# Kernel tuning notes

Measured on AMD Instinct MI355X. Metric: run time of the kernel, lower is better.

## Reference

```python
import jax, jax.numpy as jnp
import numpy as np

B, S, H, F, V, MAX_OOV = 128, 512, 1024, 512, 50000, 50


def setup_inputs() -> dict:
    key = jax.random.key(0)
    ks = jax.random.split(key, 20)
    r = lambda i, shp, s=0.02: (jax.random.normal(ks[i], shp, jnp.float32) * s)
    return dict(
        input=jax.random.randint(ks[0], (B,), 0, V),
        hidden=jax.random.normal(ks[1], (1, B, H), jnp.float32) * 0.1,
        encoder_outputs=jax.random.normal(ks[2], (B, S, H), jnp.float32) * 0.1,
        x_padding_masks=jnp.ones((B, S), jnp.float32),
        len_oov=jax.random.randint(ks[3], (B,), 0, MAX_OOV),
        coverage_vector=jnp.zeros((B, S), jnp.float32),
        ref2tgt=jax.random.randint(ks[4], (B, S), 0, V + MAX_OOV),
        emb=r(5, (V, F)),
        W_ih=r(6, (3 * H, F)), W_hh=r(7, (3 * H, H)),
        b_ih=jnp.zeros(3 * H, jnp.float32), b_hh=jnp.zeros(3 * H, jnp.float32),
        e2v1_w=r(8, (F, H)), e2v1_b=jnp.zeros(F, jnp.float32),
        e2v2_w=r(9, (V, F)), e2v2_b=jnp.zeros(V, jnp.float32),
        fc_w=r(10, (H, 2 * H)), fc_b=jnp.zeros(H, jnp.float32),
        wgen_w=r(11, (1, 2 * H + F)), wgen_b=jnp.zeros(1, jnp.float32),
        att_Wh=r(12, (H, H)), att_Ws=r(13, (H, H)),
        att_wc=r(14, (H,)), att_b=jnp.zeros(H, jnp.float32), att_v=r(15, (H,)),
    )


def reference(input, hidden, encoder_outputs, x_padding_masks, len_oov,
              coverage_vector, ref2tgt, emb, W_ih, W_hh, b_ih, b_hh,
              e2v1_w, e2v1_b, e2v2_w, e2v2_b, fc_w, fc_b, wgen_w, wgen_b,
              att_Wh, att_Ws, att_wc, att_b, att_v):
    # embedding lookup (dropout is identity at inference)
    emb_x = emb[input]  # [B, F]

    # --- additive (Bahdanau) attention with coverage ---
    s = hidden[0]  # [B, H] (n_layers == 1)
    feat = jnp.tanh(
        jnp.einsum('bsh,kh->bsk', encoder_outputs, att_Wh)
        + (s @ att_Ws.T)[:, None, :]
        + coverage_vector[:, :, None] * att_wc
        + att_b)  # [B, S, H]
    e = jnp.einsum('bsh,h->bs', feat, att_v)  # [B, S]
    a = jax.nn.softmax(e, axis=1) * x_padding_masks
    a = a / (jnp.sum(a, axis=1, keepdims=True))  # [B, S] renormalized attn
    coverage_new = coverage_vector + a
    context = jnp.einsum('bs,bsh->bh', a, encoder_outputs)  # [B, H]
    h_att = jnp.concatenate([s, context], axis=-1) @ fc_w.T + fc_b  # [B, H]

    # --- single-step GRU (PyTorch gate order r, z, n) ---
    gi = emb_x @ W_ih.T + b_ih  # [B, 3H]
    gh = h_att @ W_hh.T + b_hh  # [B, 3H]
    i_r, i_z, i_n = jnp.split(gi, 3, axis=-1)
    h_r, h_z, h_n = jnp.split(gh, 3, axis=-1)
    r = jax.nn.sigmoid(i_r + h_r)
    z = jax.nn.sigmoid(i_z + h_z)
    n = jnp.tanh(i_n + r * h_n)
    h_new = (1.0 - z) * n + z * h_att  # [B, H]

    # --- vocab distribution ---
    out1 = h_new @ e2v1_w.T + e2v1_b  # [B, F]
    p_vocab = jax.nn.softmax(out1 @ e2v2_w.T + e2v2_b, axis=1)  # [B, V]

    # --- pointer-generator mixing ---
    x_gen = jnp.concatenate([context, h_new, emb_x], axis=-1)  # [B, 2H+F]
    p_gen = jax.nn.sigmoid(x_gen @ wgen_w.T + wgen_b)[:, 0]  # [B]
    p_gen = jnp.clip(p_gen, 0.001, 0.999)
    p_vocab_w = p_gen[:, None] * p_vocab  # [B, V]
    attn_w = (1.0 - p_gen)[:, None] * a  # [B, S]
    p_ext = jnp.concatenate([p_vocab_w, jnp.zeros((B, MAX_OOV), p_vocab_w.dtype)], axis=1)
    rows = jnp.arange(B)[:, None]
    final = p_ext.at[rows, ref2tgt].add(attn_w)  # scatter_add over extended vocab

    return final, h_new[None], coverage_new, a
```

## Files before the change

### kernel.cpp

```cpp
#include <hip/hip_runtime.h>
#include <math.h>

#define B_   128
#define S_   512
#define H_   1024
#define F_   512
#define V_   50000
#define OOV_ 50
#define EV_  (V_ + OOV_)

#define BM 128
#define BN 128
#define BK 64

#define BM2 256
#define BN2 256
#define BK2 64

typedef __attribute__((ext_vector_type(8))) __bf16 bf16x8;
typedef __attribute__((ext_vector_type(4))) __bf16 bf16x4;
typedef __attribute__((ext_vector_type(4))) float  f32x4;

__device__ __forceinline__ void gload_lds16(const void* g, void* lds) {
  __builtin_amdgcn_global_load_lds(
      (const __attribute__((address_space(1))) unsigned int*)g,
      (__attribute__((address_space(3))) unsigned int*)lds, 16, 0, 0);
}

__device__ __forceinline__ float fast_tanh(float x) {
  float v = fminf(fmaxf(x, -15.f), 15.f);
  float t = __expf(2.f * v);
  return 1.f - 2.f / (t + 1.f);
}

__global__ __launch_bounds__(256)
void cast_both_kernel(const float* __restrict__ enc, __bf16* __restrict__ enc_h,
                      const float* __restrict__ wh, __bf16* __restrict__ wh_h)
{
  const size_t n_enc = (size_t)B_ * S_ * H_;
  const size_t n_tot = n_enc + (size_t)H_ * H_;
  for (size_t i = ((size_t)blockIdx.x * 256 + threadIdx.x) * 8; i < n_tot;
       i += (size_t)gridDim.x * 256 * 8) {
    const float* in; __bf16* out; size_t j;
    if (i < n_enc) { in = enc; out = enc_h; j = i; }
    else           { in = wh;  out = wh_h;  j = i - n_enc; }
    float4 a = *(const float4*)(in + j);
    float4 b = *(const float4*)(in + j + 4);
    bf16x8 o;
    o[0] = (__bf16)a.x; o[1] = (__bf16)a.y; o[2] = (__bf16)a.z; o[3] = (__bf16)a.w;
    o[4] = (__bf16)b.x; o[5] = (__bf16)b.y; o[6] = (__bf16)b.z; o[7] = (__bf16)b.w;
    *(bf16x8*)(out + j) = o;
  }
}

__global__ __launch_bounds__(256)
void gemm_splitk(const float* __restrict__ A, const float* __restrict__ W,
                 float* __restrict__ partial, int N, int K, int KS)
{
  __shared__ float As[128 * 68];
  __shared__ float Ws[32 * 68];
  const int tid = threadIdx.x;
  const int n0 = blockIdx.x * 32;
  const int p  = blockIdx.y;
  const int tx = tid & 7, ty = tid >> 3;
  const int lr = tid >> 4, lc4 = (tid & 15) * 4;
  float acc[4][4] = {};
  const int kend = p * KS + KS;
  for (int k0 = p * KS; k0 < kend; k0 += 64) {
#pragma unroll
    for (int pp = 0; pp < 8; ++pp)
      *(float4*)(As + (pp * 16 + lr) * 68 + lc4) =
          *(const float4*)(A + (size_t)(pp * 16 + lr) * K + k0 + lc4);
#pragma unroll
    for (int pp = 0; pp < 2; ++pp)
      *(float4*)(Ws + (pp * 16 + lr) * 68 + lc4) =
          *(const float4*)(W + (size_t)(n0 + pp * 16 + lr) * K + k0 + lc4);
    __syncthreads();
#pragma unroll
    for (int kk = 0; kk < 16; ++kk) {
      float4 av[4], wv[4];
#pragma unroll
      for (int i = 0; i < 4; i++) av[i] = *(const float4*)(As + (ty * 4 + i) * 68 + kk * 4);
#pragma unroll
      for (int j = 0; j < 4; j++) wv[j] = *(const float4*)(Ws + (tx * 4 + j) * 68 + kk * 4);
#pragma unroll
      for (int i = 0; i < 4; i++)
#pragma unroll
        for (int j = 0; j < 4; j++) {
          acc[i][j] = fmaf(av[i].x, wv[j].x, acc[i][j]);
          acc[i][j] = fmaf(av[i].y, wv[j].y, acc[i][j]);
          acc[i][j] = fmaf(av[i].z, wv[j].z, acc[i][j]);
          acc[i][j] = fmaf(av[i].w, wv[j].w, acc[i][j]);
        }
    }
    __syncthreads();
  }
#pragma unroll
  for (int i = 0; i < 4; i++)
#pragma unroll
    for (int j = 0; j < 4; j++)
      partial[((size_t)p * 128 + ty * 4 + i) * N + n0 + tx * 4 + j] = acc[i][j];
}

__global__ __launch_bounds__(256)
void gemm_splitk_cat(const float* __restrict__ A1, const float* __restrict__ A2,
                     const float* __restrict__ W, float* __restrict__ partial,
                     int N, int K, int KS)
{
  __shared__ float As[128 * 68];
  __shared__ float Ws[32 * 68];
  const int tid = threadIdx.x;
  const int n0 = blockIdx.x * 32;
  const int p  = blockIdx.y;
  const int tx = tid & 7, ty = tid >> 3;
  const int lr = tid >> 4, lc4 = (tid & 15) * 4;
  const float* A = (p * KS < 1024) ? A1 : A2;
  const int kbase = (p * KS < 1024) ? 0 : 1024;
  float acc[4][4] = {};
  const int kend = p * KS + KS;
  for (int k0 = p * KS; k0 < kend; k0 += 64) {
#pragma unroll
    for (int pp = 0; pp < 8; ++pp)
      *(float4*)(As + (pp * 16 + lr) * 68 + lc4) =
          *(const float4*)(A + (size_t)(pp * 16 + lr) * 1024 + (k0 - kbase) + lc4);
#pragma unroll
    for (int pp = 0; pp < 2; ++pp)
      *(float4*)(Ws + (pp * 16 + lr) * 68 + lc4) =
          *(const float4*)(W + (size_t)(n0 + pp * 16 + lr) * K + k0 + lc4);
    __syncthreads();
#pragma unroll
    for (int kk = 0; kk < 16; ++kk) {
      float4 av[4], wv[4];
#pragma unroll
      for (int i = 0; i < 4; i++) av[i] = *(const float4*)(As + (ty * 4 + i) * 68 + kk * 4);
#pragma unroll
      for (int j = 0; j < 4; j++) wv[j] = *(const float4*)(Ws + (tx * 4 + j) * 68 + kk * 4);
#pragma unroll
      for (int i = 0; i < 4; i++)
#pragma unroll
        for (int j = 0; j < 4; j++) {
          acc[i][j] = fmaf(av[i].x, wv[j].x, acc[i][j]);
          acc[i][j] = fmaf(av[i].y, wv[j].y, acc[i][j]);
          acc[i][j] = fmaf(av[i].z, wv[j].z, acc[i][j]);
          acc[i][j] = fmaf(av[i].w, wv[j].w, acc[i][j]);
        }
    }
    __syncthreads();
  }
#pragma unroll
  for (int i = 0; i < 4; i++)
#pragma unroll
    for (int j = 0; j < 4; j++)
      partial[((size_t)p * 128 + ty * 4 + i) * N + n0 + tx * 4 + j] = acc[i][j];
}

__global__ __launch_bounds__(256)
void gemm_splitk_gather(const int* __restrict__ input, const float* __restrict__ emb,
                        const float* __restrict__ W, float* __restrict__ partial,
                        int N, int K, int KS)
{
  __shared__ float As[128 * 68];
  __shared__ float Ws[32 * 68];
  const int tid = threadIdx.x;
  const int n0 = blockIdx.x * 32;
  const int p  = blockIdx.y;
  const int tx = tid & 7, ty = tid >> 3;
  const int lr = tid >> 4, lc4 = (tid & 15) * 4;
  float acc[4][4] = {};
  const int kend = p * KS + KS;
  for (int k0 = p * KS; k0 < kend; k0 += 64) {
#pragma unroll
    for (int pp = 0; pp < 8; ++pp) {
      int row = input[pp * 16 + lr];
      *(float4*)(As + (pp * 16 + lr) * 68 + lc4) =
          *(const float4*)(emb + (size_t)row * K + k0 + lc4);
    }
#pragma unroll
    for (int pp = 0; pp < 2; ++pp)
      *(float4*)(Ws + (pp * 16 + lr) * 68 + lc4) =
          *(const float4*)(W + (size_t)(n0 + pp * 16 + lr) * K + k0 + lc4);
    __syncthreads();
#pragma unroll
    for (int kk = 0; kk < 16; ++kk) {
      float4 av[4], wv[4];
#pragma unroll
      for (int i = 0; i < 4; i++) av[i] = *(const float4*)(As + (ty * 4 + i) * 68 + kk * 4);
#pragma unroll
      for (int j = 0; j < 4; j++) wv[j] = *(const float4*)(Ws + (tx * 4 + j) * 68 + kk * 4);
#pragma unroll
      for (int i = 0; i < 4; i++)
#pragma unroll
        for (int j = 0; j < 4; j++) {
          acc[i][j] = fmaf(av[i].x, wv[j].x, acc[i][j]);
          acc[i][j] = fmaf(av[i].y, wv[j].y, acc[i][j]);
          acc[i][j] = fmaf(av[i].z, wv[j].z, acc[i][j]);
          acc[i][j] = fmaf(av[i].w, wv[j].w, acc[i][j]);
        }
    }
    __syncthreads();
  }
#pragma unroll
  for (int i = 0; i < 4; i++)
#pragma unroll
    for (int j = 0; j < 4; j++)
      partial[((size_t)p * 128 + ty * 4 + i) * N + n0 + tx * 4 + j] = acc[i][j];
}

__global__ __launch_bounds__(256)
void reduce_partial(const float* __restrict__ partial, const float* __restrict__ bias,
                    float* __restrict__ C, int N, int P)
{
  int idx = blockIdx.x * 256 + threadIdx.x;
  int n = idx % N;
  float s = bias ? bias[n] : 0.f;
  for (int p = 0; p < P; ++p) s += partial[(size_t)p * 128 * N + idx];
  C[idx] = s;
}

__global__ __launch_bounds__(256)
void reduce_partial_bf16(const float* __restrict__ partial, const float* __restrict__ bias,
                         __bf16* __restrict__ C, int N, int P)
{
  int idx = blockIdx.x * 256 + threadIdx.x;
  int n = idx % N;
  float s = bias ? bias[n] : 0.f;
  for (int p = 0; p < P; ++p) s += partial[(size_t)p * 128 * N + idx];
  C[idx] = (__bf16)s;
}

__global__ __launch_bounds__(512, 1)
void feat_mfma256_kernel(const __bf16* __restrict__ enc, const __bf16* __restrict__ Wh,
                         const float* __restrict__ sws, const float* __restrict__ cov,
                         const float* __restrict__ wcv, const float* __restrict__ ab,
                         const float* __restrict__ av_, float* __restrict__ e_part)
{
  __shared__ __attribute__((aligned(16))) __bf16 As[2][BM2 * BK2];
  __shared__ __attribute__((aligned(16))) __bf16 Bs[2][BN2 * BK2];
  const int tid  = threadIdx.x;
  const int lane = tid & 63, wid = tid >> 6;
  const int wr = wid >> 2, wc = wid & 3;
  const int bid = blockIdx.x;
  const int swz = (bid & 7) * 128 + (bid >> 3);
  const int mt = swz >> 2, nt = swz & 3;
  const int bs0 = mt * BM2;
  const int n0  = nt * BN2;
  const int b   = bs0 >> 9;

  const int scb = ((tid & 7) * 16) ^ (((tid >> 3) & 7) << 4);
  const __bf16* aP[4]; const __bf16* bP[4]; int ldsO[4];
#pragma unroll
  for (int p = 0; p < 4; ++p) {
    int r = p * 64 + (tid >> 3);
    ldsO[p] = p * 8192 + tid * 16;
    aP[p] = enc + (size_t)(bs0 + r) * H_ + (scb >> 1);
    bP[p] = Wh  + (size_t)(n0  + r) * H_ + (scb >> 1);
  }

  const int lrow = lane & 15;
  const int kbase = (lane >> 4) << 4;
  int aO[8][2], bO[4][2];
#pragma unroll
  for (int m = 0; m < 8; ++m) {
    int row = wr * 128 + m * 16 + lrow;
    int sw = (row & 7) << 4;
#pragma unroll
    for (int kk = 0; kk < 2; ++kk)
      aO[m][kk] = row * 128 + ((kk * 64 + kbase) ^ sw);
  }
#pragma unroll
  for (int n = 0; n < 4; ++n) {
    int row = wc * 64 + n * 16 + lrow;
    int sw = (row & 7) << 4;
#pragma unroll
    for (int kk = 0; kk < 2; ++kk)
      bO[n][kk] = row * 128 + ((kk * 64 + kbase) ^ sw);
  }

  f32x4 acc[8][4];
#pragma unroll
  for (int i = 0; i < 8; i++)
#pragma unroll
    for (int j = 0; j < 4; j++) acc[i][j] = (f32x4){0.f, 0.f, 0.f, 0.f};

#define STAGE(c, ofs)                                                          \
  {                                                                            \
    _Pragma("unroll")                                                          \
    for (int p = 0; p < 4; ++p) {                                              \
      gload_lds16(aP[p] + (ofs), (char*)As[c] + ldsO[p]);                      \
      gload_lds16(bP[p] + (ofs), (char*)Bs[c] + ldsO[p]);                      \
    }                                                                          \
  }

#define COMPUTE(c)                                                             \
  {                                                                            \
    bf16x8 bfv[4][2];                                                          \
    _Pragma("unroll")                                                          \
    for (int n = 0; n < 4; ++n)                                                \
      _Pragma("unroll")                                                        \
      for (int kk = 0; kk < 2; ++kk)                                           \
        bfv[n][kk] = *(const bf16x8*)((const char*)Bs[c] + bO[n][kk]);         \
    __builtin_amdgcn_s_setprio(1);                                             \
    _Pragma("unroll")                                                          \
    for (int m = 0; m < 8; ++m) {                                              \
      bf16x8 a0 = *(const bf16x8*)((const char*)As[c] + aO[m][0]);             \
      bf16x8 a1 = *(const bf16x8*)((const char*)As[c] + aO[m][1]);             \
      _Pragma("unroll")                                                        \
      for (int n = 0; n < 4; ++n) {                                            \
        acc[m][n] = __builtin_amdgcn_mfma_f32_16x16x32_bf16(a0, bfv[n][0], acc[m][n], 0, 0, 0); \
        acc[m][n] = __builtin_amdgcn_mfma_f32_16x16x32_bf16(a1, bfv[n][1], acc[m][n], 0, 0, 0); \
      }                                                                        \
    }                                                                          \
    __builtin_amdgcn_s_setprio(0);                                             \
  }

#define VMCNT8() asm volatile("s_waitcnt vmcnt(8)" ::: "memory")
#define VMCNT0() asm volatile("s_waitcnt vmcnt(0)" ::: "memory")
#define BARRIER()                                                              \
  {                                                                            \
    __builtin_amdgcn_sched_barrier(0);                                         \
    __builtin_amdgcn_s_barrier();                                              \
    __builtin_amdgcn_sched_barrier(0);                                         \
  }

  STAGE(0, 0)
  STAGE(1, 64)

#pragma unroll 1
  for (int t2 = 0; t2 < 7; ++t2) {
    VMCNT8(); BARRIER();
    COMPUTE(0)
    BARRIER();
    STAGE(0, 128)
    VMCNT8(); BARRIER();
    COMPUTE(1)
    BARRIER();
    STAGE(1, 192)
#pragma unroll
    for (int p = 0; p < 4; ++p) { aP[p] += 128; bP[p] += 128; }
  }
  VMCNT8(); BARRIER();
  COMPUTE(0)
  BARRIER();
  VMCNT0(); BARRIER();
  COMPUTE(1)
  __syncthreads();
#undef STAGE
#undef COMPUTE
#undef VMCNT8
#undef VMCNT0
#undef BARRIER

  float rowsum[8][4];
#pragma unroll
  for (int m = 0; m < 8; m++)
#pragma unroll
    for (int j = 0; j < 4; j++) rowsum[m][j] = 0.f;

#pragma unroll
  for (int n = 0; n < 4; ++n) {
    int col_g = n0 + wc * 64 + n * 16 + (lane & 15);
    float sw   = sws[(size_t)b * H_ + col_g];
    float wc_n = wcv[col_g], ab_n = ab[col_g], av_n = av_[col_g];
#pragma unroll
    for (int m = 0; m < 8; ++m) {
#pragma unroll
      for (int j = 0; j < 4; ++j) {
        int row_l = wr * 128 + m * 16 + ((lane >> 4) << 2) + j;
        float val = acc[m][n][j] + sw + cov[bs0 + row_l] * wc_n + ab_n;
        rowsum[m][j] += fast_tanh(val) * av_n;
      }
    }
  }
#pragma unroll
  for (int m = 0; m < 8; ++m)
#pragma unroll
    for (int j = 0; j < 4; ++j) {
      float v = rowsum[m][j];
      v += __shfl_xor(v, 1);
      v += __shfl_xor(v, 2);
      v += __shfl_xor(v, 4);
      v += __shfl_xor(v, 8);
      rowsum[m][j] = v;
    }
  float (*red)[4] = (float(*)[4])As;
  if ((lane & 15) == 0) {
#pragma unroll
    for (int m = 0; m < 8; ++m)
#pragma unroll
      for (int j = 0; j < 4; ++j)
        red[wr * 128 + m * 16 + ((lane >> 4) << 2) + j][wc] = rowsum[m][j];
  }
  __syncthreads();
  if (tid < BM2)
    e_part[(size_t)nt * (B_ * S_) + bs0 + tid] =
        red[tid][0] + red[tid][1] + red[tid][2] + red[tid][3];
}

__global__ __launch_bounds__(256)
void logits_mfma_kernel(const __bf16* __restrict__ A, const float* __restrict__ W,
                        const float* __restrict__ bias, float* __restrict__ out0)
{
  __shared__ __attribute__((aligned(16))) __bf16 As[BM * BK];
  __shared__ __attribute__((aligned(16))) __bf16 Bs[BN * BK];
  const int tid  = threadIdx.x;
  const int lane = tid & 63, wid = tid >> 6;
  const int wr = wid >> 1, wcc = wid & 1;
  const int n0 = blockIdx.x * BN;

  f32x4 acc[4][4];
#pragma unroll
  for (int i = 0; i < 4; i++)
#pragma unroll
    for (int j = 0; j < 4; j++) acc[i][j] = (f32x4){0.f, 0.f, 0.f, 0.f};

  for (int k0 = 0; k0 < F_; k0 += BK) {
#pragma unroll
    for (int p = 0; p < 4; ++p) {
      int off = p * 4096 + tid * 16;
      int r = off >> 7, cb = off & 127;
      int scb = cb ^ ((r & 7) << 4);
      gload_lds16(A + (size_t)r * F_ + k0 + (scb >> 1), (char*)As + off);
    }
#pragma unroll
    for (int p = 0; p < 8; ++p) {
      int idx = p * 1024 + tid * 4;
      int r = idx >> 6, c = idx & 63;
      int row_g = n0 + r; if (row_g >= V_) row_g = V_ - 1;
      float4 f = *(const float4*)(W + (size_t)row_g * F_ + k0 + c);
      union { __bf16 h[4]; uint2 u; } t;
      t.h[0] = (__bf16)f.x; t.h[1] = (__bf16)f.y; t.h[2] = (__bf16)f.z; t.h[3] = (__bf16)f.w;
      int cb = c * 2;
      *(uint2*)((char*)Bs + r * 128 + (cb ^ ((r & 7) << 4))) = t.u;
    }
    __syncthreads();

    bf16x8 af[4][2], bfv[4][2];
#pragma unroll
    for (int m = 0; m < 4; ++m) {
      int row = wr * 64 + m * 16 + (lane & 15);
      int swz = (row & 7) << 4;
#pragma unroll
      for (int kk = 0; kk < 2; ++kk) {
        int kb = kk * 64 + ((lane >> 4) << 4);
        af[m][kk] = *(const bf16x8*)((const char*)As + row * 128 + (kb ^ swz));
      }
    }
#pragma unroll
    for (int n = 0; n < 4; ++n) {
      int row = wcc * 64 + n * 16 + (lane & 15);
      int swz = (row & 7) << 4;
#pragma unroll
      for (int kk = 0; kk < 2; ++kk) {
        int kb = kk * 64 + ((lane >> 4) << 4);
        bfv[n][kk] = *(const bf16x8*)((const char*)Bs + row * 128 + (kb ^ swz));
      }
    }
#pragma unroll
    for (int m = 0; m < 4; ++m)
#pragma unroll
      for (int n = 0; n < 4; ++n)
#pragma unroll
        for (int kk = 0; kk < 2; ++kk)
          acc[m][n] = __builtin_amdgcn_mfma_f32_16x16x32_bf16(af[m][kk], bfv[n][kk], acc[m][n], 0, 0, 0);
    __syncthreads();
  }

#pragma unroll
  for (int m = 0; m < 4; ++m) {
#pragma unroll
    for (int n = 0; n < 4; ++n) {
      int col_g = n0 + wcc * 64 + n * 16 + (lane & 15);
      if (col_g >= V_) continue;
      float bv = bias[col_g];
#pragma unroll
      for (int j = 0; j < 4; ++j) {
        int row = wr * 64 + m * 16 + ((lane >> 4) << 2) + j;
        out0[(size_t)row * EV_ + col_g] = acc[m][n][j] + bv;
      }
    }
  }
}

__global__ __launch_bounds__(512)
void softmax_a_kernel(const float* __restrict__ e_part, const float* __restrict__ mask,
                      const float* __restrict__ cov, float* __restrict__ a_ws,
                      float* __restrict__ out_a, float* __restrict__ out_cov)
{
  const int b = blockIdx.x;
  const int s = threadIdx.x;
  __shared__ float red[512];
  float e = 0.f;
  for (int kt = 0; kt < 4; ++kt) e += e_part[(size_t)kt * (B_ * S_) + b * S_ + s];
  red[s] = e;
  __syncthreads();
  for (int st = 256; st > 0; st >>= 1) {
    if (s < st) red[s] = fmaxf(red[s], red[s + st]);
    __syncthreads();
  }
  float mx = red[0];
  __syncthreads();
  float ex = expf(e - mx) * mask[b * S_ + s];
  red[s] = ex;
  __syncthreads();
  for (int st = 256; st > 0; st >>= 1) {
    if (s < st) red[s] += red[s + st];
    __syncthreads();
  }
  float a = ex / red[0];
  a_ws[b * S_ + s] = a;
  out_a[b * S_ + s] = a;
  out_cov[b * S_ + s] = cov[b * S_ + s] + a;
}

__global__ __launch_bounds__(256)
void context_kernel(const float* __restrict__ a_ws, const __bf16* __restrict__ enc,
                    float* __restrict__ ctx)
{
  const int b = blockIdx.y, q = blockIdx.x;
  const int lane = threadIdx.x & 63, w = threadIdx.x >> 6;
  const int h0 = q * 256 + lane * 4;
  __shared__ float al[S_];
  __shared__ float part[4][256];
  for (int i = threadIdx.x; i < S_; i += 256) al[i] = a_ws[b * S_ + i];
  __syncthreads();
  float acc0 = 0.f, acc1 = 0.f, acc2 = 0.f, acc3 = 0.f;
  const __bf16* ep = enc + (size_t)b * S_ * H_ + h0;
#pragma unroll 4
  for (int s = w * 128; s < w * 128 + 128; ++s) {
    bf16x4 v = *(const bf16x4*)(ep + (size_t)s * H_);
    float a = al[s];
    acc0 = fmaf(a, (float)v[0], acc0);
    acc1 = fmaf(a, (float)v[1], acc1);
    acc2 = fmaf(a, (float)v[2], acc2);
    acc3 = fmaf(a, (float)v[3], acc3);
  }
  part[w][lane * 4 + 0] = acc0;
  part[w][lane * 4 + 1] = acc1;
  part[w][lane * 4 + 2] = acc2;
  part[w][lane * 4 + 3] = acc3;
  __syncthreads();
  if (threadIdx.x < 256) {
    int o = threadIdx.x;
    ctx[b * H_ + q * 256 + o] = part[0][o] + part[1][o] + part[2][o] + part[3][o];
  }
}

__global__ __launch_bounds__(256)
void gru_kernel(const float* __restrict__ pgi, const float* __restrict__ pgh,
                const float* __restrict__ b_ih, const float* __restrict__ b_hh,
                const float* __restrict__ h_att, float* __restrict__ h_new_ws,
                float* __restrict__ out_h)
{
  int idx = blockIdx.x * 256 + threadIdx.x;
  int b = idx >> 10, h = idx & 1023;
  float ir = b_ih[h], iz = b_ih[H_ + h], in_ = b_ih[2 * H_ + h];
  float hr = b_hh[h], hz = b_hh[H_ + h], hn = b_hh[2 * H_ + h];
#pragma unroll
  for (int p = 0; p < 8; ++p) {
    const float* gp = pgi + (size_t)p * 128 * 3072 + (size_t)b * 3072;
    ir += gp[h]; iz += gp[H_ + h]; in_ += gp[2 * H_ + h];
    const float* hp = pgh + (size_t)p * 128 * 3072 + (size_t)b * 3072;
    hr += hp[h]; hz += hp[H_ + h]; hn += hp[2 * H_ + h];
  }
  float r = 1.f / (1.f + expf(-(ir + hr)));
  float z = 1.f / (1.f + expf(-(iz + hz)));
  float n = tanhf(in_ + r * hn);
  float ha = h_att[(size_t)b * H_ + h];
  float hv = (1.f - z) * n + z * ha;
  h_new_ws[idx] = hv;
  out_h[idx] = hv;
}

__global__ __launch_bounds__(512)
void stats_pgen_kernel(const float* __restrict__ logits, float* __restrict__ vmax,
                       float* __restrict__ vsum, const float* __restrict__ context,
                       const float* __restrict__ h_new, const int* __restrict__ input,
                       const float* __restrict__ emb, const float* __restrict__ wgen_w,
                       const float* __restrict__ wgen_b, float* __restrict__ pgen)
{
  __shared__ float red[512];
  if (blockIdx.x < B_) {
    int b = blockIdx.x;
    const float* row = logits + (size_t)b * EV_;
    float m = -1e30f;
    for (int v = threadIdx.x; v < V_; v += 512) m = fmaxf(m, row[v]);
    red[threadIdx.x] = m;
    __syncthreads();
    for (int st = 256; st > 0; st >>= 1) {
      if (threadIdx.x < st) red[threadIdx.x] = fmaxf(red[threadIdx.x], red[threadIdx.x + st]);
      __syncthreads();
    }
    m = red[0];
    __syncthreads();
    float ssum = 0.f;
    for (int v = threadIdx.x; v < V_; v += 512) ssum += expf(row[v] - m);
    red[threadIdx.x] = ssum;
    __syncthreads();
    for (int st = 256; st > 0; st >>= 1) {
      if (threadIdx.x < st) red[threadIdx.x] += red[threadIdx.x + st];
      __syncthreads();
    }
    if (threadIdx.x == 0) { vmax[b] = m; vsum[b] = red[0]; }
  } else {
    int b = blockIdx.x - B_;
    const float* erow = emb + (size_t)input[b] * F_;
    float acc = 0.f;
    for (int j = threadIdx.x; j < H_; j += 512) acc = fmaf(context[b * H_ + j], wgen_w[j], acc);
    for (int j = threadIdx.x; j < H_; j += 512) acc = fmaf(h_new[b * H_ + j], wgen_w[H_ + j], acc);
    for (int j = threadIdx.x; j < F_; j += 512) acc = fmaf(erow[j], wgen_w[2 * H_ + j], acc);
    red[threadIdx.x] = acc;
    __syncthreads();
    for (int st = 256; st > 0; st >>= 1) {
      if (threadIdx.x < st) red[threadIdx.x] += red[threadIdx.x + st];
      __syncthreads();
    }
    if (threadIdx.x == 0) {
      float p = 1.f / (1.f + expf(-(red[0] + wgen_b[0])));
      p = fminf(fmaxf(p, 0.001f), 0.999f);
      pgen[b] = p;
    }
  }
}

__global__ void final_kernel(float* __restrict__ out0, const float* __restrict__ vmax,
                             const float* __restrict__ vsum, const float* __restrict__ pgen)
{
  int b = blockIdx.y;
  int v = blockIdx.x * 256 + threadIdx.x;
  if (v >= EV_) return;
  float* row = out0 + (size_t)b * EV_;
  if (v < V_) row[v] = pgen[b] * expf(row[v] - vmax[b]) / vsum[b];
  else row[v] = 0.f;
}

__global__ void scatter_kernel(const int* __restrict__ ref2tgt, const float* __restrict__ a_ws,
                               const float* __restrict__ pgen, float* __restrict__ out0)
{
  int b = blockIdx.x;
  int s = threadIdx.x;
  float w = (1.f - pgen[b]) * a_ws[b * S_ + s];
  int t = ref2tgt[b * S_ + s];
  atomicAdd(&out0[(size_t)b * EV_ + t], w);
}

extern "C" void kernel_launch(void* const* d_in, const int* in_sizes, int n_in,
                              void* d_out, int out_size, void* d_ws, size_t ws_size,
                              hipStream_t stream)
{
  const int*   input   = (const int*)d_in[0];
  const float* hidden  = (const float*)d_in[1];
  const float* enc     = (const float*)d_in[2];
  const float* mask    = (const float*)d_in[3];
  const float* cov     = (const float*)d_in[5];
  const int*   ref2tgt = (const int*)d_in[6];
  const float* emb     = (const float*)d_in[7];
  const float* W_ih    = (const float*)d_in[8];
  const float* W_hh    = (const float*)d_in[9];
  const float* b_ih    = (const float*)d_in[10];
  const float* b_hh    = (const float*)d_in[11];
  const float* e2v1_w  = (const float*)d_in[12];
  const float* e2v1_b  = (const float*)d_in[13];
  const float* e2v2_w  = (const float*)d_in[14];
  const float* e2v2_b  = (const float*)d_in[15];
  const float* fc_w    = (const float*)d_in[16];
  const float* fc_b    = (const float*)d_in[17];
  const float* wgen_w  = (const float*)d_in[18];
  const float* wgen_b  = (const float*)d_in[19];
  const float* att_Wh  = (const float*)d_in[20];
  const float* att_Ws  = (const float*)d_in[21];
  const float* att_wc  = (const float*)d_in[22];
  const float* att_b   = (const float*)d_in[23];
  const float* att_v   = (const float*)d_in[24];

  char* w = (char*)d_ws;
  __bf16* enc_h  = (__bf16*)w;  w += (size_t)B_ * S_ * H_ * 2;
  __bf16* Wh_h   = (__bf16*)w;  w += (size_t)H_ * H_ * 2;
  __bf16* out1_h = (__bf16*)w;  w += (size_t)B_ * F_ * 2;
  float* sws     = (float*)w;   w += (size_t)B_ * H_ * 4;
  float* e_part  = (float*)w;   w += (size_t)8 * B_ * S_ * 4;
  float* a_ws    = (float*)w;   w += (size_t)B_ * S_ * 4;
  float* context = (float*)w;   w += (size_t)B_ * H_ * 4;
  float* h_att   = (float*)w;   w += (size_t)B_ * H_ * 4;
  float* h_new   = (float*)w;   w += (size_t)B_ * H_ * 4;
  float* pgen    = (float*)w;   w += 128 * 4;
  float* vmax    = (float*)w;   w += 128 * 4;
  float* vsum    = (float*)w;   w += 128 * 4;
  float* pA      = (float*)w;   w += (size_t)16 * 128 * 1024 * 4;
  float* pB      = (float*)w;   w += (size_t)8 * 128 * 3072 * 4;
  float* pC      = (float*)w;   w += (size_t)8 * 128 * 3072 * 4;

  float* out0    = (float*)d_out;
  float* out_h   = out0 + (size_t)B_ * EV_;
  float* out_cov = out_h + (size_t)B_ * H_;
  float* out_a   = out_cov + (size_t)B_ * S_;

  cast_both_kernel<<<4096, 256, 0, stream>>>(enc, enc_h, att_Wh, Wh_h);
  gemm_splitk<<<dim3(32, 16), 256, 0, stream>>>(hidden, att_Ws, pA, H_, H_, 64);
  reduce_partial<<<512, 256, 0, stream>>>(pA, nullptr, sws, H_, 16);
  feat_mfma256_kernel<<<dim3(1024), 512, 0, stream>>>(enc_h, Wh_h, sws, cov, att_wc, att_b, att_v, e_part);
  softmax_a_kernel<<<B_, 512, 0, stream>>>(e_part, mask, cov, a_ws, out_a, out_cov);
  context_kernel<<<dim3(4, B_), 256, 0, stream>>>(a_ws, enc_h, context);
  gemm_splitk_cat<<<dim3(32, 16), 256, 0, stream>>>(hidden, context, fc_w, pA, H_, 2 * H_, 128);
  reduce_partial<<<512, 256, 0, stream>>>(pA, fc_b, h_att, H_, 16);
  gemm_splitk_gather<<<dim3(96, 8), 256, 0, stream>>>(input, emb, W_ih, pB, 3 * H_, F_, 64);
  gemm_splitk<<<dim3(96, 8), 256, 0, stream>>>(h_att, W_hh, pC, 3 * H_, H_, 128);
  gru_kernel<<<(B_ * H_) / 256, 256, 0, stream>>>(pB, pC, b_ih, b_hh, h_att, h_new, out_h);
  gemm_splitk<<<dim3(16, 16), 256, 0, stream>>>(h_new, e2v1_w, pA, F_, H_, 64);
  reduce_partial_bf16<<<256, 256, 0, stream>>>(pA, e2v1_b, out1_h, F_, 16);
  logits_mfma_kernel<<<dim3((V_ + BN - 1) / BN), 256, 0, stream>>>(out1_h, e2v2_w, e2v2_b, out0);
  stats_pgen_kernel<<<2 * B_, 512, 0, stream>>>(out0, vmax, vsum, context, h_new, input, emb,
                                                wgen_w, wgen_b, pgen);
  final_kernel<<<dim3((EV_ + 255) / 256, B_), 256, 0, stream>>>(out0, vmax, vsum, pgen);
  scatter_kernel<<<B_, 512, 0, stream>>>(ref2tgt, a_ws, pgen, out0);
}
```

Baseline: 484.0 us.

## Split feat GEMM K-loop into fine-grained phases interleaving loads with MFMA

Restructures the attention-feature GEMM main loop into an HipKittens-style 8-phase schedule. LDS tiles are split into half-tiles, and each phase issues one small global->LDS stage, reads A fragments, then runs 16 MFMAs. The goal is to spread memory traffic evenly across compute and hide load latency better than the previous two-big-stage double buffer. It adds more barriers and lgkm waits per K step, and the handling of buffer reuse between phases is delicate.

```diff
diff --git a/kernel.cpp b/kernel.cpp
--- a/kernel.cpp
+++ b/kernel.cpp
@@ -12,10 +12,6 @@
 #define BM 128
 #define BN 128
 #define BK 64
-
-#define BM2 256
-#define BN2 256
-#define BK2 64
 
 typedef __attribute__((ext_vector_type(8))) __bf16 bf16x8;
 typedef __attribute__((ext_vector_type(4))) __bf16 bf16x4;
@@ -234,46 +230,45 @@
                          const float* __restrict__ wcv, const float* __restrict__ ab,
                          const float* __restrict__ av_, float* __restrict__ e_part)
 {
-  __shared__ __attribute__((aligned(16))) __bf16 As[2][BM2 * BK2];
-  __shared__ __attribute__((aligned(16))) __bf16 Bs[2][BN2 * BK2];
+  __shared__ __attribute__((aligned(16))) __bf16 As[2][2][128 * 64];
+  __shared__ __attribute__((aligned(16))) __bf16 Bs[2][2][128 * 64];
   const int tid  = threadIdx.x;
   const int lane = tid & 63, wid = tid >> 6;
   const int wr = wid >> 2, wc = wid & 3;
   const int bid = blockIdx.x;
   const int swz = (bid & 7) * 128 + (bid >> 3);
   const int mt = swz >> 2, nt = swz & 3;
-  const int bs0 = mt * BM2;
-  const int n0  = nt * BN2;
+  const int bs0 = mt * 256;
+  const int n0  = nt * 256;
   const int b   = bs0 >> 9;
 
   const int scb = ((tid & 7) * 16) ^ (((tid >> 3) & 7) << 4);
-  const __bf16* aP[4]; const __bf16* bP[4]; int ldsO[4];
-#pragma unroll
-  for (int p = 0; p < 4; ++p) {
-    int r = p * 64 + (tid >> 3);
-    ldsO[p] = p * 8192 + tid * 16;
-    aP[p] = enc + (size_t)(bs0 + r) * H_ + (scb >> 1);
-    bP[p] = Wh  + (size_t)(n0  + r) * H_ + (scb >> 1);
-  }
-
-  const int lrow = lane & 15;
-  const int kbase = (lane >> 4) << 4;
+  const __bf16* aS[2][2];
+  const __bf16* bS[2][2];
+#pragma unroll
+  for (int h = 0; h < 2; ++h)
+#pragma unroll
+    for (int q = 0; q < 2; ++q) {
+      int r = h * 128 + q * 64 + (tid >> 3);
+      aS[h][q] = enc + (size_t)(bs0 + r) * H_ + (scb >> 1);
+      bS[h][q] = Wh  + (size_t)(n0  + r) * H_ + (scb >> 1);
+    }
+  const int ldsQ0 = tid * 16, ldsQ1 = 8192 + tid * 16;
+
+  const int lrow = lane & 15, kbase = (lane >> 4) << 4;
+  const int bh = wc >> 1;
   int aO[8][2], bO[4][2];
 #pragma unroll
   for (int m = 0; m < 8; ++m) {
-    int row = wr * 128 + m * 16 + lrow;
-    int sw = (row & 7) << 4;
-#pragma unroll
-    for (int kk = 0; kk < 2; ++kk)
-      aO[m][kk] = row * 128 + ((kk * 64 + kbase) ^ sw);
+    int rh = m * 16 + lrow, sw = (rh & 7) << 4;
+    aO[m][0] = rh * 128 + (kbase ^ sw);
+    aO[m][1] = rh * 128 + ((64 + kbase) ^ sw);
   }
 #pragma unroll
   for (int n = 0; n < 4; ++n) {
-    int row = wc * 64 + n * 16 + lrow;
-    int sw = (row & 7) << 4;
-#pragma unroll
-    for (int kk = 0; kk < 2; ++kk)
-      bO[n][kk] = row * 128 + ((kk * 64 + kbase) ^ sw);
+    int rh = (wc & 1) * 64 + n * 16 + lrow, sw = (rh & 7) << 4;
+    bO[n][0] = rh * 128 + (kbase ^ sw);
+    bO[n][1] = rh * 128 + ((64 + kbase) ^ sw);
   }
 
   f32x4 acc[8][4];
@@ -281,74 +276,88 @@
   for (int i = 0; i < 8; i++)
 #pragma unroll
     for (int j = 0; j < 4; j++) acc[i][j] = (f32x4){0.f, 0.f, 0.f, 0.f};
-
-#define STAGE(c, ofs)                                                          \
+  bf16x8 bfv[4][2];
+
+#define STG_A(d, h, ofs)                                                       \
+  { gload_lds16(aS[h][0] + (ofs), (char*)As[d][h] + ldsQ0);                    \
+    gload_lds16(aS[h][1] + (ofs), (char*)As[d][h] + ldsQ1); }
+#define STG_B(d, h, ofs)                                                       \
+  { gload_lds16(bS[h][0] + (ofs), (char*)Bs[d][h] + ldsQ0);                    \
+    gload_lds16(bS[h][1] + (ofs), (char*)Bs[d][h] + ldsQ1); }
+#define BAR()                                                                  \
+  { __builtin_amdgcn_sched_barrier(0); __builtin_amdgcn_s_barrier();           \
+    __builtin_amdgcn_sched_barrier(0); }
+#define LGKM0()                                                                \
+  { asm volatile("s_waitcnt lgkmcnt(0)" ::: "memory");                         \
+    __builtin_amdgcn_sched_barrier(0); }
+#define VMC(n)                                                                 \
+  { asm volatile("s_waitcnt vmcnt(" #n ")" ::: "memory");                      \
+    __builtin_amdgcn_sched_barrier(0); }
+#define RD_B(d)                                                                \
+  { _Pragma("unroll")                                                          \
+    for (int n = 0; n < 4; ++n) {                                              \
+      bfv[n][0] = *(const bf16x8*)((const char*)Bs[d][bh] + bO[n][0]);         \
+      bfv[n][1] = *(const bf16x8*)((const char*)Bs[d][bh] + bO[n][1]);         \
+    } }
+#define PH(d, q, STGSTMT, TAILWAIT)                                            \
   {                                                                            \
-    _Pragma("unroll")                                                          \
-    for (int p = 0; p < 4; ++p) {                                              \
-      gload_lds16(aP[p] + (ofs), (char*)As[c] + ldsO[p]);                      \
-      gload_lds16(bP[p] + (ofs), (char*)Bs[c] + ldsO[p]);                      \
-    }                                                                          \
-  }
-
-#define COMPUTE(c)                                                             \
-  {                                                                            \
-    bf16x8 bfv[4][2];                                                          \
-    _Pragma("unroll")                                                          \
-    for (int n = 0; n < 4; ++n)                                                \
-      _Pragma("unroll")                                                        \
-      for (int kk = 0; kk < 2; ++kk)                                           \
-        bfv[n][kk] = *(const bf16x8*)((const char*)Bs[c] + bO[n][kk]);         \
+    bf16x8 x00 = *(const bf16x8*)((const char*)As[d][wr] + aO[2*(q)][0]);      \
+    bf16x8 x01 = *(const bf16x8*)((const char*)As[d][wr] + aO[2*(q)][1]);      \
+    bf16x8 x10 = *(const bf16x8*)((const char*)As[d][wr] + aO[2*(q)+1][0]);    \
+    bf16x8 x11 = *(const bf16x8*)((const char*)As[d][wr] + aO[2*(q)+1][1]);    \
+    STGSTMT;                                                                   \
+    BAR(); LGKM0();                                                            \
     __builtin_amdgcn_s_setprio(1);                                             \
     _Pragma("unroll")                                                          \
-    for (int m = 0; m < 8; ++m) {                                              \
-      bf16x8 a0 = *(const bf16x8*)((const char*)As[c] + aO[m][0]);             \
-      bf16x8 a1 = *(const bf16x8*)((const char*)As[c] + aO[m][1]);             \
-      _Pragma("unroll")                                                        \
-      for (int n = 0; n < 4; ++n) {                                            \
-        acc[m][n] = __builtin_amdgcn_mfma_f32_16x16x32_bf16(a0, bfv[n][0], acc[m][n], 0, 0, 0); \
-        acc[m][n] = __builtin_amdgcn_mfma_f32_16x16x32_bf16(a1, bfv[n][1], acc[m][n], 0, 0, 0); \
-      }                                                                        \
+    for (int n = 0; n < 4; ++n) {                                              \
+      acc[2*(q)][n]   = __builtin_amdgcn_mfma_f32_16x16x32_bf16(x00, bfv[n][0], acc[2*(q)][n], 0, 0, 0);   \
+      acc[2*(q)][n]   = __builtin_amdgcn_mfma_f32_16x16x32_bf16(x01, bfv[n][1], acc[2*(q)][n], 0, 0, 0);   \
+      acc[2*(q)+1][n] = __builtin_amdgcn_mfma_f32_16x16x32_bf16(x10, bfv[n][0], acc[2*(q)+1][n], 0, 0, 0); \
+      acc[2*(q)+1][n] = __builtin_amdgcn_mfma_f32_16x16x32_bf16(x11, bfv[n][1], acc[2*(q)+1][n], 0, 0, 0); \
     }                                                                          \
     __builtin_amdgcn_s_setprio(0);                                             \
-  }
-
-#define VMCNT8() asm volatile("s_waitcnt vmcnt(8)" ::: "memory")
-#define VMCNT0() asm volatile("s_waitcnt vmcnt(0)" ::: "memory")
-#define BARRIER()                                                              \
-  {                                                                            \
-    __builtin_amdgcn_sched_barrier(0);                                         \
-    __builtin_amdgcn_s_barrier();                                              \
-    __builtin_amdgcn_sched_barrier(0);                                         \
-  }
-
-  STAGE(0, 0)
-  STAGE(1, 64)
+    TAILWAIT; BAR();                                                           \
+  }
+
+  STG_B(0, 0, 0) STG_B(0, 1, 0) STG_A(0, 0, 0) STG_A(0, 1, 0)
+  STG_B(1, 0, 64) STG_B(1, 1, 64)
+  VMC(4); BAR();
 
 #pragma unroll 1
-  for (int t2 = 0; t2 < 7; ++t2) {
-    VMCNT8(); BARRIER();
-    COMPUTE(0)
-    BARRIER();
-    STAGE(0, 128)
-    VMCNT8(); BARRIER();
-    COMPUTE(1)
-    BARRIER();
-    STAGE(1, 192)
-#pragma unroll
-    for (int p = 0; p < 4; ++p) { aP[p] += 128; bP[p] += 128; }
-  }
-  VMCNT8(); BARRIER();
-  COMPUTE(0)
-  BARRIER();
-  VMCNT0(); BARRIER();
-  COMPUTE(1)
+  for (int i = 0; i < 7; ++i) {
+    RD_B(0);
+    PH(0, 0, STG_A(1, 0, 64), )
+    PH(0, 1, STG_A(1, 1, 64), )
+    PH(0, 2, STG_B(0, 0, 128), )
+    PH(0, 3, STG_B(0, 1, 128), VMC(4))
+    RD_B(1);
+    PH(1, 0, STG_A(0, 0, 128), )
+    PH(1, 1, STG_A(0, 1, 128), )
+    PH(1, 2, STG_B(1, 0, 192), )
+    PH(1, 3, STG_B(1, 1, 192), VMC(4))
+#pragma unroll
+    for (int h = 0; h < 2; ++h)
+#pragma unroll
+      for (int q = 0; q < 2; ++q) { aS[h][q] += 128; bS[h][q] += 128; }
+  }
+  RD_B(0);
+  PH(0, 0, STG_A(1, 0, 64), )
+  PH(0, 1, STG_A(1, 1, 64), )
+  PH(0, 2, , )
+  PH(0, 3, , VMC(0))
+  RD_B(1);
+  PH(1, 0, , )
+  PH(1, 1, , )
+  PH(1, 2, , )
+  PH(1, 3, , )
   __syncthreads();
-#undef STAGE
-#undef COMPUTE
-#undef VMCNT8
-#undef VMCNT0
-#undef BARRIER
+#undef STG_A
+#undef STG_B
+#undef BAR
+#undef LGKM0
+#undef VMC
+#undef RD_B
+#undef PH
 
   float rowsum[8][4];
 #pragma unroll
@@ -391,7 +400,7 @@
         red[wr * 128 + m * 16 + ((lane >> 4) << 2) + j][wc] = rowsum[m][j];
   }
   __syncthreads();
-  if (tid < BM2)
+  if (tid < 256)
     e_part[(size_t)nt * (B_ * S_) + bs0 + tid] =
         red[tid][0] + red[tid][1] + red[tid][2] + red[tid][3];
 }
```

Measured after the change: 461.1 us. 4.7% less time.
